# Kernel tuning notes

Measured on AMD Instinct MI355X. Metric: run time of the kernel, lower is better.

Reference implementation:

```python
import jax, jax.numpy as jnp
import numpy as np

B, S, H, T = 64, 512, 768, 9


def setup_inputs() -> dict:
    key = jax.random.key(0)
    ks = jax.random.split(key, 8)
    embeddings = jax.random.normal(ks[0], (B, S, H), dtype=jnp.float32)
    # variable-length mask (first token always valid), as token_type_ids would give
    lengths = jax.random.randint(ks[1], (B,), 1, S + 1)
    mask = (jnp.arange(S)[None, :] < lengths[:, None]).astype(jnp.int32)
    labels = jax.random.randint(ks[2], (B, S), 0, T)
    W = jax.random.normal(ks[3], (T, H), dtype=jnp.float32) * (1.0 / np.sqrt(H))
    b = jnp.zeros((T,), dtype=jnp.float32)
    start_trans = jax.random.normal(ks[4], (T,), dtype=jnp.float32) * 0.1
    transitions = jax.random.normal(ks[5], (T, T), dtype=jnp.float32) * 0.1
    end_trans = jax.random.normal(ks[6], (T,), dtype=jnp.float32) * 0.1
    return {"embeddings": embeddings, "W": W, "b": b,
            "start_trans": start_trans, "transitions": transitions,
            "end_trans": end_trans, "labels": labels, "mask": mask}


def _crf_nll(emissions, labels, mask_bool, start_trans, transitions, end_trans):
    # emissions: [B,S,T]; returns negative log-likelihood per sequence [B]
    Bn = emissions.shape[0]
    mask_f = mask_bool.astype(emissions.dtype)
    # --- gold path score (numerator) ---
    first = start_trans[labels[:, 0]] + emissions[jnp.arange(Bn), 0, labels[:, 0]]
    emis_sc = jnp.take_along_axis(emissions, labels[..., None], axis=2)[..., 0]  # [B,S]
    trans_sc = transitions[labels[:, :-1], labels[:, 1:]]                         # [B,S-1]
    num = first + jnp.sum((emis_sc[:, 1:] + trans_sc) * mask_f[:, 1:], axis=1)
    last_idx = jnp.sum(mask_bool.astype(jnp.int32), axis=1) - 1
    last_lab = jnp.take_along_axis(labels, last_idx[:, None], axis=1)[:, 0]
    num = num + end_trans[last_lab]
    # --- log partition (forward algorithm, logsumexp recurrence) ---
    alpha0 = start_trans[None, :] + emissions[:, 0]          # [B,T]
    em_t = jnp.swapaxes(emissions, 0, 1)[1:]                 # [S-1,B,T]
    m_t = mask_bool.T[1:]                                    # [S-1,B]
    def step(alpha, xs):
        em, m = xs
        new = jax.nn.logsumexp(alpha[:, :, None] + transitions[None], axis=1) + em
        return jnp.where(m[:, None], new, alpha), None
    alpha, _ = jax.lax.scan(step, alpha0, (em_t, m_t))
    denom = jax.nn.logsumexp(alpha + end_trans[None, :], axis=1)
    return denom - num


def reference(embeddings, W, b, start_trans, transitions, end_trans, labels, mask):
    # dropout is identity at eval; Linear + ReLU emissions
    emissions = jax.nn.relu(jnp.einsum('bsh,th->bst', embeddings, W) + b)
    # -100 padding handling: zero out mask there, clamp labels to 0
    valid = labels != -100
    mask_bool = (mask != 0) & valid
    labels_mod = jnp.where(valid, labels, 0)
    nll = _crf_nll(emissions, labels_mod, mask_bool, start_trans, transitions, end_trans)
    return jnp.mean(nll)  # == -loss.mean() of the log-likelihood
```

## Files before the change

### kernel.cpp

```cpp
#include <hip/hip_runtime.h>

#define NEG_INF (-1e30f)

static constexpr int Bn = 64;
static constexpr int Sn = 512;
static constexpr int Hn = 768;
static constexpr int Tn = 9;
static constexpr int KC = 32;
static constexpr int CL = 16;
static constexpr int PSTRIDE = 108;

__device__ __forceinline__ float dot4(float4 a, float4 b) {
    return a.x * b.x + a.y * b.y + a.z * b.z + a.w * b.w;
}

__global__ __launch_bounds__(256) void emis_kernel(const float* __restrict__ emb,
        const float* __restrict__ Wm, const float* __restrict__ bias,
        float* __restrict__ em) {
    const int lane = threadIdx.x & 63;
    const int gw = (blockIdx.x * 256 + threadIdx.x) >> 6;
    const int nw = (gridDim.x * 256) >> 6;
    const int NP = (Bn * Sn) >> 1;

    float4 w[Tn][3];
#pragma unroll
    for (int t = 0; t < Tn; ++t) {
        const float4* w4 = (const float4*)(Wm + t * Hn);
#pragma unroll
        for (int i = 0; i < 3; ++i) w[t][i] = w4[lane + (i << 6)];
    }
    float bb[Tn];
#pragma unroll
    for (int t = 0; t < Tn; ++t) bb[t] = bias[t];

    const int sub = (lane < 9) ? lane : (lane - 9);

    float4 cA0, cA1, cA2, cB0, cB1, cB2;
    int p = gw;
    if (p < NP) {
        const float4* a4 = (const float4*)(emb + (size_t)(2 * p) * Hn);
        cA0 = a4[lane]; cA1 = a4[lane + 64]; cA2 = a4[lane + 128];
        cB0 = a4[lane + 192]; cB1 = a4[lane + 256]; cB2 = a4[lane + 320];
    }
    while (p < NP) {
        const int pn = p + nw;
        float4 nA0, nA1, nA2, nB0, nB1, nB2;
        if (pn < NP) {
            const float4* a4 = (const float4*)(emb + (size_t)(2 * pn) * Hn);
            nA0 = a4[lane]; nA1 = a4[lane + 64]; nA2 = a4[lane + 128];
            nB0 = a4[lane + 192]; nB1 = a4[lane + 256]; nB2 = a4[lane + 320];
        }
        float accA[Tn], accB[Tn];
#pragma unroll
        for (int t = 0; t < Tn; ++t) {
            accA[t] = dot4(cA0, w[t][0]) + dot4(cA1, w[t][1]) + dot4(cA2, w[t][2]);
            accB[t] = dot4(cB0, w[t][0]) + dot4(cB1, w[t][1]) + dot4(cB2, w[t][2]);
        }
#pragma unroll
        for (int off = 32; off; off >>= 1) {
#pragma unroll
            for (int t = 0; t < Tn; ++t) {
                accA[t] += __shfl_xor(accA[t], off);
                accB[t] += __shfl_xor(accB[t], off);
            }
        }
        float outv = 0.0f;
#pragma unroll
        for (int t = 0; t < Tn; ++t) {
            float va = fmaxf(accA[t] + bb[t], 0.0f);
            float vb = fmaxf(accB[t] + bb[t], 0.0f);
            float sel = (lane < 9) ? va : vb;
            outv = (sub == t) ? sel : outv;
        }
        if (lane < 18) em[(size_t)(2 * p) * Tn + lane] = outv;
        p = pn;
        cA0 = nA0; cA1 = nA1; cA2 = nA2;
        cB0 = nB0; cB1 = nB1; cB2 = nB2;
    }
}

__global__ __launch_bounds__(128) void chunk_kernel(const float* __restrict__ em,
        const float* __restrict__ trans, const int* __restrict__ labels,
        const int* __restrict__ mask, float* __restrict__ chunkP,
        float* __restrict__ auxN, int* __restrict__ auxC) {
    const int bk = blockIdx.x;
    const int b  = bk >> 5;
    const int k  = bk & 31;
    const int t0 = 1 + k * CL;
    const int tid  = threadIdx.x;
    const int w    = tid >> 6;
    const int lane = tid & 63;

    __shared__ float em_s[CL][Tn];
    __shared__ int   on_s[CL];
    __shared__ float tr_s[81];

    if (tid < 81) tr_s[tid] = trans[tid];

    int myLab = 0, myLabP = 0, myOn = 0;
    if (tid < CL) {
        int t = t0 + tid;
        if (t < Sn) {
            int lb = labels[b * Sn + t];
            int lp = labels[b * Sn + t - 1];
            int mm = mask[b * Sn + t];
            myOn  = (mm != 0) && (lb != -100);
            myLab = (lb == -100) ? 0 : lb;
            myLabP = (lp == -100) ? 0 : lp;
        }
        on_s[tid] = myOn;
    }
    {
        const int nst = (Sn - t0 < CL) ? (Sn - t0) : CL;
        const float* src = em + (size_t)(b * Sn + t0) * Tn;
        for (int u = tid; u < nst * Tn; u += 128) ((float*)em_s)[u] = src[u];
    }
    __syncthreads();

    float nump = 0.0f;
    int cnt = 0;
    if (tid < CL && myOn) {
        nump = em_s[tid][myLab] + tr_s[myLabP * Tn + myLab];
        cnt = 1;
    }
    if (w == 0) {
#pragma unroll
        for (int off = 8; off; off >>= 1) {
            nump += __shfl_xor(nump, off);
            cnt  += __shfl_xor(cnt, off);
        }
        if (lane == 0) { auxN[bk] = nump; auxC[bk] = cnt; }
    }

    const int v  = lane / 9;
    const int jj = lane - v * 9;
    const bool act = lane < ((w == 0) ? 45 : 36);
    const int rid = (w == 0) ? v : (5 + v);

    float c[Tn];
#pragma unroll
    for (int kk = 0; kk < Tn; ++kk) c[kk] = tr_s[kk * Tn + jj];

    float pv = (act && rid == jj) ? 0.0f : NEG_INF;

    for (int u = 0; u < CL; ++u) {
        if (!on_s[u]) continue;
        float x[Tn];
#pragma unroll
        for (int kk = 0; kk < Tn; ++kk) {
            float a = __shfl(pv, (v * Tn + kk) & 63);
            x[kk] = a + c[kk];
        }
        float mx = x[0];
#pragma unroll
        for (int kk = 1; kk < Tn; ++kk) mx = fmaxf(mx, x[kk]);
        float s = 0.0f;
#pragma unroll
        for (int kk = 0; kk < Tn; ++kk) s += __expf(x[kk] - mx);
        float nv = mx + __logf(s) + em_s[u][jj];
        pv = act ? nv : pv;
    }
    if (act) chunkP[(size_t)bk * PSTRIDE + jj * 12 + rid] = pv;
}

__global__ __launch_bounds__(64) void combine_kernel(const float* __restrict__ em,
        const float* __restrict__ startT, const float* __restrict__ endT,
        const int* __restrict__ labels, const int* __restrict__ mask,
        const float* __restrict__ chunkP, const float* __restrict__ auxN,
        const int* __restrict__ auxC, float* __restrict__ nll) {
    const int b = blockIdx.x;
    const int lane = threadIdx.x;

    float em0 = (lane < Tn) ? em[(size_t)b * Sn * Tn + lane] : NEG_INF;
    float alpha = (lane < Tn) ? (startT[lane] + em0) : NEG_INF;

    int lab0r = labels[b * Sn];
    int lab0 = (lab0r == -100) ? 0 : lab0r;
    float first = startT[lab0] + __shfl(em0, lab0);

    float numP = (lane < KC) ? auxN[b * KC + lane] : 0.0f;
    int   cntP = (lane < KC) ? auxC[b * KC + lane] : 0;
#pragma unroll
    for (int off = 32; off; off >>= 1) {
        numP += __shfl_xor(numP, off);
        cntP += __shfl_xor(cntP, off);
    }
    int m0 = ((mask[b * Sn] != 0) && (lab0r != -100)) ? 1 : 0;
    int cntTot = cntP + m0;
    int lastIdx = cntTot - 1;
    if (lastIdx < 0) lastIdx = 0;
    int lastLab = labels[b * Sn + lastIdx];
    lastLab = (lastLab == -100) ? 0 : lastLab;
    float num = first + numP + endT[lastLab];

    const float* Pb = chunkP + (size_t)b * KC * PSTRIDE;
    float4 p0 = make_float4(0, 0, 0, 0), p1 = p0, p2 = p0;
    if (lane < Tn) {
        const float4* pp = (const float4*)(Pb + lane * 12);
        p0 = pp[0]; p1 = pp[1]; p2 = pp[2];
    }
    for (int k = 0; k < KC; ++k) {
        float4 q0 = p0, q1 = p1, q2 = p2;
        if (k + 1 < KC && lane < Tn) {
            const float4* pp = (const float4*)(Pb + (size_t)(k + 1) * PSTRIDE + lane * 12);
            p0 = pp[0]; p1 = pp[1]; p2 = pp[2];
        }
        float av[Tn];
#pragma unroll
        for (int i = 0; i < Tn; ++i) av[i] = __shfl(alpha, i);
        float x[Tn];
        x[0] = av[0] + q0.x; x[1] = av[1] + q0.y; x[2] = av[2] + q0.z;
        x[3] = av[3] + q0.w; x[4] = av[4] + q1.x; x[5] = av[5] + q1.y;
        x[6] = av[6] + q1.z; x[7] = av[7] + q1.w; x[8] = av[8] + q2.x;
        float mx = x[0];
#pragma unroll
        for (int i = 1; i < Tn; ++i) mx = fmaxf(mx, x[i]);
        float s = 0.0f;
#pragma unroll
        for (int i = 0; i < Tn; ++i) s += __expf(x[i] - mx);
        float na = mx + __logf(s);
        alpha = (lane < Tn) ? na : NEG_INF;
    }

    float z = (lane < Tn) ? (alpha + endT[lane]) : NEG_INF;
    float mx = z;
#pragma unroll
    for (int off = 32; off; off >>= 1) mx = fmaxf(mx, __shfl_xor(mx, off));
    float s = __expf(z - mx);
#pragma unroll
    for (int off = 32; off; off >>= 1) s += __shfl_xor(s, off);
    float denom = mx + __logf(s);

    if (lane == 0) nll[b] = denom - num;
}

__global__ __launch_bounds__(64) void mean_kernel(const float* __restrict__ nll,
        float* __restrict__ out) {
    float v = nll[threadIdx.x];
#pragma unroll
    for (int off = 32; off; off >>= 1) v += __shfl_xor(v, off);
    if (threadIdx.x == 0) out[0] = v * (1.0f / 64.0f);
}

extern "C" void kernel_launch(void* const* d_in, const int* in_sizes, int n_in,
                              void* d_out, int out_size, void* d_ws, size_t ws_size,
                              hipStream_t stream) {
    const float* emb    = (const float*)d_in[0];
    const float* Wm     = (const float*)d_in[1];
    const float* bias   = (const float*)d_in[2];
    const float* startT = (const float*)d_in[3];
    const float* trans  = (const float*)d_in[4];
    const float* endT   = (const float*)d_in[5];
    const int*   labels = (const int*)d_in[6];
    const int*   mask   = (const int*)d_in[7];

    float* em     = (float*)d_ws;
    float* chunkP = em + (size_t)Bn * Sn * Tn;
    float* auxN   = chunkP + (size_t)Bn * KC * PSTRIDE;
    int*   auxC   = (int*)(auxN + (size_t)Bn * KC);
    float* nll    = (float*)(auxC + (size_t)Bn * KC);
    float* out    = (float*)d_out;

    emis_kernel<<<768, 256, 0, stream>>>(emb, Wm, bias, em);
    chunk_kernel<<<Bn * KC, 128, 0, stream>>>(em, trans, labels, mask,
                                              chunkP, auxN, auxC);
    combine_kernel<<<Bn, 64, 0, stream>>>(em, startT, endT, labels, mask,
                                          chunkP, auxN, auxC, nll);
    mean_kernel<<<1, 64, 0, stream>>>(nll, out);
}
```

Before: 68.99 us.

## Restructure emission GEMV so each lane owns a row with K-split across waves

After: 60.30 us. 1.14x faster.

```diff
diff --git a/kernel.cpp b/kernel.cpp
--- a/kernel.cpp
+++ b/kernel.cpp
@@ -14,68 +14,43 @@
     return a.x * b.x + a.y * b.y + a.z * b.z + a.w * b.w;
 }
 
-__global__ __launch_bounds__(256) void emis_kernel(const float* __restrict__ emb,
+__global__ __launch_bounds__(512) void emis_kernel(const float* __restrict__ emb,
         const float* __restrict__ Wm, const float* __restrict__ bias,
         float* __restrict__ em) {
-    const int lane = threadIdx.x & 63;
-    const int gw = (blockIdx.x * 256 + threadIdx.x) >> 6;
-    const int nw = (gridDim.x * 256) >> 6;
-    const int NP = (Bn * Sn) >> 1;
-
-    float4 w[Tn][3];
-#pragma unroll
-    for (int t = 0; t < Tn; ++t) {
-        const float4* w4 = (const float4*)(Wm + t * Hn);
-#pragma unroll
-        for (int i = 0; i < 3; ++i) w[t][i] = w4[lane + (i << 6)];
-    }
-    float bb[Tn];
-#pragma unroll
-    for (int t = 0; t < Tn; ++t) bb[t] = bias[t];
-
-    const int sub = (lane < 9) ? lane : (lane - 9);
-
-    float4 cA0, cA1, cA2, cB0, cB1, cB2;
-    int p = gw;
-    if (p < NP) {
-        const float4* a4 = (const float4*)(emb + (size_t)(2 * p) * Hn);
-        cA0 = a4[lane]; cA1 = a4[lane + 64]; cA2 = a4[lane + 128];
-        cB0 = a4[lane + 192]; cB1 = a4[lane + 256]; cB2 = a4[lane + 320];
-    }
-    while (p < NP) {
-        const int pn = p + nw;
-        float4 nA0, nA1, nA2, nB0, nB1, nB2;
-        if (pn < NP) {
-            const float4* a4 = (const float4*)(emb + (size_t)(2 * pn) * Hn);
-            nA0 = a4[lane]; nA1 = a4[lane + 64]; nA2 = a4[lane + 128];
-            nB0 = a4[lane + 192]; nB1 = a4[lane + 256]; nB2 = a4[lane + 320];
-        }
-        float accA[Tn], accB[Tn];
+    const int blk  = blockIdx.x;
+    const int tid  = threadIdx.x;
+    const int lane = tid & 63;
+    const int seg  = __builtin_amdgcn_readfirstlane(tid >> 6);
+    const int row  = blk * 64 + lane;
+
+    __shared__ float part[8][64][Tn];
+
+    const float4* e4 = (const float4*)emb + (size_t)row * 192 + seg * 24;
+    const float4* w4 = (const float4*)Wm;
+
+    float acc[Tn];
+#pragma unroll
+    for (int t = 0; t < Tn; ++t) acc[t] = 0.0f;
+
+#pragma unroll 4
+    for (int i = 0; i < 24; ++i) {
+        float4 e = e4[i];
 #pragma unroll
         for (int t = 0; t < Tn; ++t) {
-            accA[t] = dot4(cA0, w[t][0]) + dot4(cA1, w[t][1]) + dot4(cA2, w[t][2]);
-            accB[t] = dot4(cB0, w[t][0]) + dot4(cB1, w[t][1]) + dot4(cB2, w[t][2]);
-        }
-#pragma unroll
-        for (int off = 32; off; off >>= 1) {
-#pragma unroll
-            for (int t = 0; t < Tn; ++t) {
-                accA[t] += __shfl_xor(accA[t], off);
-                accB[t] += __shfl_xor(accB[t], off);
-            }
-        }
-        float outv = 0.0f;
-#pragma unroll
-        for (int t = 0; t < Tn; ++t) {
-            float va = fmaxf(accA[t] + bb[t], 0.0f);
-            float vb = fmaxf(accB[t] + bb[t], 0.0f);
-            float sel = (lane < 9) ? va : vb;
-            outv = (sub == t) ? sel : outv;
-        }
-        if (lane < 18) em[(size_t)(2 * p) * Tn + lane] = outv;
-        p = pn;
-        cA0 = nA0; cA1 = nA1; cA2 = nA2;
-        cB0 = nB0; cB1 = nB1; cB2 = nB2;
+            float4 wt = w4[t * 192 + seg * 24 + i];
+            acc[t] += dot4(e, wt);
+        }
+    }
+#pragma unroll
+    for (int t = 0; t < Tn; ++t) part[seg][lane][t] = acc[t];
+    __syncthreads();
+
+    for (int o = tid; o < 64 * Tn; o += 512) {
+        int r = o / Tn, t = o - r * Tn;
+        float s = 0.0f;
+#pragma unroll
+        for (int sg = 0; sg < 8; ++sg) s += part[sg][r][t];
+        em[(size_t)blk * (64 * Tn) + o] = fmaxf(s + bias[t], 0.0f);
     }
 }
 
@@ -261,7 +236,7 @@
     float* nll    = (float*)(auxC + (size_t)Bn * KC);
     float* out    = (float*)d_out;
 
-    emis_kernel<<<768, 256, 0, stream>>>(emb, Wm, bias, em);
+    emis_kernel<<<Bn * Sn / 64, 512, 0, stream>>>(emb, Wm, bias, em);
     chunk_kernel<<<Bn * KC, 128, 0, stream>>>(em, trans, labels, mask,
                                               chunkP, auxN, auxC);
     combine_kernel<<<Bn, 64, 0, stream>>>(em, startT, endT, labels, mask,
```
